# Optimization experiments

Hardware: AMD Instinct MI355X
Metric: run time of the kernel (lower is better)

## Reference

```python
import jax, jax.numpy as jnp
import numpy as np
from jax import lax

LATENT = 64
NUM_EMB = 512
BETA = 0.25
DN = ('NCHW', 'OIHW', 'NCHW')


def conv(x, w, b, stride, pad):
    y = lax.conv_general_dilated(x, w, (stride, stride), [(pad, pad), (pad, pad)],
                                 dimension_numbers=DN)
    return y + b[None, :, None, None]


def tconv(x, w, b, stride, pad, opad):
    # torch ConvTranspose2d(k=3, stride, padding=pad, output_padding=opad)
    # == dilated conv with lhs_dilation=stride, padding (k-1-pad, k-1-pad+opad),
    #    spatially-flipped kernel. w is stored OIHW (out, in, kh, kw).
    k = w.shape[2]
    lo, hi = k - 1 - pad, k - 1 - pad + opad
    y = lax.conv_general_dilated(x, w[:, :, ::-1, ::-1], (1, 1), [(lo, hi), (lo, hi)],
                                 lhs_dilation=(stride, stride), dimension_numbers=DN)
    return y + b[None, :, None, None]


def vector_quantize(z, codebook):
    # z: (B, D, H, W); codebook: (K, D)
    B, D, H, W = z.shape
    flat = z.transpose(0, 2, 3, 1).reshape(-1, D)  # (BHW, D)
    d = (jnp.sum(flat ** 2, axis=1, keepdims=True)
         + jnp.sum(codebook ** 2, axis=1)
         - 2.0 * flat @ codebook.T)  # (BHW, K)
    idx = jnp.argmin(d, axis=1)
    q = codebook[idx].reshape(B, H, W, D).transpose(0, 3, 1, 2)  # (B, D, H, W)
    commitment = jnp.mean((lax.stop_gradient(q) - z) ** 2)
    codebook_loss = jnp.mean((q - lax.stop_gradient(z)) ** 2)
    loss = BETA * commitment + codebook_loss
    q_ste = z + lax.stop_gradient(q - z)  # straight-through estimator
    return q_ste, loss


def setup_inputs() -> dict:
    key = jax.random.key(0)
    ks = jax.random.split(key, 16)
    f32 = jnp.float32
    inp = {
        'x': jax.random.uniform(ks[0], (1024, 1, 50, 50), dtype=f32),
        'enc_w1': jax.random.normal(ks[1], (32, 1, 3, 3), f32) * 0.1,
        'enc_b1': jnp.zeros((32,), f32),
        'enc_w2': jax.random.normal(ks[2], (64, 32, 3, 3), f32) * 0.05,
        'enc_b2': jnp.zeros((64,), f32),
        'enc_w3': jax.random.normal(ks[3], (LATENT, 64, 1, 1), f32) * 0.1,
        'enc_b3': jnp.zeros((LATENT,), f32),
        'codebook': jax.random.uniform(ks[4], (NUM_EMB, LATENT), dtype=f32),
        'dec_w1': jax.random.normal(ks[5], (64, LATENT, 3, 3), f32) * 0.05,
        'dec_b1': jnp.zeros((64,), f32),
        'dec_w2': jax.random.normal(ks[6], (32, 64, 3, 3), f32) * 0.05,
        'dec_b2': jnp.zeros((32,), f32),
        'dec_w3': jax.random.normal(ks[7], (1, 32, 3, 3), f32) * 0.05,
        'dec_b3': jnp.zeros((1,), f32),
    }
    return inp


def reference(x, enc_w1, enc_b1, enc_w2, enc_b2, enc_w3, enc_b3, codebook,
              dec_w1, dec_b1, dec_w2, dec_b2, dec_w3, dec_b3):
    # encoder: (B,1,50,50) -> (B,LATENT,13,13)
    h = jax.nn.relu(conv(x, enc_w1, enc_b1, 2, 1))
    h = jax.nn.relu(conv(h, enc_w2, enc_b2, 2, 1))
    z = conv(h, enc_w3, enc_b3, 1, 0)
    q, vq_loss = vector_quantize(z, codebook)
    # decoder: 13 -> 25 -> 50
    h = jax.nn.relu(tconv(q, dec_w1, dec_b1, 2, 1, 0))
    h = jax.nn.relu(tconv(h, dec_w2, dec_b2, 2, 1, 1))
    x_recon = jax.nn.sigmoid(conv(h, dec_w3, dec_b3, 1, 1))
    return x_recon, vq_loss
```

## Files before the change

### kernel.cpp

```cpp
#include <hip/hip_runtime.h>
#include <math.h>


typedef __attribute__((ext_vector_type(8))) short s8v;
typedef __attribute__((ext_vector_type(4))) float f4v;
typedef __attribute__((ext_vector_type(4))) int i4v;

__device__ inline unsigned short f2bf(float f) {
    unsigned u = __builtin_bit_cast(unsigned, f);
    return (unsigned short)((u + 0x7fffu + ((u >> 16) & 1u)) >> 16);
}
__device__ inline float bf2f(unsigned short h) {
    return __builtin_bit_cast(float, ((unsigned)h) << 16);
}

__global__ __launch_bounds__(64) void k_zero(float* __restrict__ p) {
    if (threadIdx.x == 0 && blockIdx.x == 0) *p = 0.f;
}

__global__ __launch_bounds__(256) void k_prep_cn(const float* __restrict__ cb,
                                                 float* __restrict__ cn) {
    int k = blockIdx.x * 256 + threadIdx.x;
    const float* r = cb + k * 64;
    float s = 0.f;
#pragma unroll
    for (int c = 0; c < 64; ++c) s += r[c] * r[c];
    cn[k] = s;
}
__global__ __launch_bounds__(256) void k_prep_cbm(const float* __restrict__ cb,
                                                  unsigned short* __restrict__ o) {
    int i = blockIdx.x * 256 + threadIdx.x;
    int j = i & 7, lane = (i >> 3) & 63;
    int kc = (i >> 9) % 6, nt = (i >> 9) / 6;
    int n = nt * 16 + (lane & 15);
    int k = kc * 32 + ((lane >> 4) << 3) + j;
    int seg = k >> 6, kk = k & 63;
    float c = cb[n * 64 + kk];
    unsigned short ch = f2bf(c);
    o[i] = (seg == 1) ? f2bf(c - bf2f(ch)) : ch;
}
__global__ __launch_bounds__(256) void k_prep_B2n(const float* __restrict__ w,
                                                  unsigned short* __restrict__ o) {
    int i = blockIdx.x * 256 + threadIdx.x;
    if (i >= 55296) return;
    int j = i & 7, lane = (i >> 3) & 63;
    int kc = (i >> 9) % 27, nt = (i >> 9) / 27;
    int k = kc * 32 + ((lane >> 4) << 3) + j;
    int co = nt * 16 + (lane & 15);
    int part = (k < 288) ? 0 : (k < 576) ? 1 : 0;
    int kk = (k < 288) ? k : (k < 576) ? k - 288 : k - 576;
    int tap = kk >> 5, ci = kk & 31;
    float v = w[(co * 32 + ci) * 9 + tap];
    unsigned short hi = f2bf(v);
    o[i] = part ? f2bf(v - bf2f(hi)) : hi;
}
__global__ __launch_bounds__(256) void k_prep_B3(const float* __restrict__ w,
                                                 unsigned short* __restrict__ o) {
    int i = blockIdx.x * 256 + threadIdx.x;
    if (i >= 12288) return;
    int j = i & 7, lane = (i >> 3) & 63;
    int kc = (i >> 9) % 6, nt = (i >> 9) / 6;
    int k = kc * 32 + ((lane >> 4) << 3) + j;
    int n = nt * 16 + (lane & 15);
    int part = (k < 64) ? 0 : (k < 128) ? 1 : 0;
    int kk = (k < 64) ? k : (k < 128) ? k - 64 : k - 128;
    float v = w[n * 64 + kk];
    unsigned short hi = f2bf(v);
    o[i] = part ? f2bf(v - bf2f(hi)) : hi;
}
__global__ __launch_bounds__(256) void k_prep_B1(const float* __restrict__ w,
                                                 unsigned short* __restrict__ o) {
    int i = blockIdx.x * 256 + threadIdx.x;
    int j = i & 7, l = (i >> 3) & 63, kc = (i >> 9) & 7, nt = i >> 12;
    int n = nt * 16 + (l & 15), k = kc * 32 + (l >> 4) * 8 + j;
    int cls = n >> 6, co = n & 63, p = k >> 6, ci = k & 63;
    int jh = -1, jw = -1;
    if (cls == 0)      { if (p == 0) { jh = 1; jw = 1; } }
    else if (cls == 1) { if (p == 1) { jh = 1; jw = 0; } else if (p == 0) { jh = 1; jw = 2; } }
    else if (cls == 2) { if (p == 2) { jh = 0; jw = 1; } else if (p == 0) { jh = 2; jw = 1; } }
    else { if (p == 3) { jh = 0; jw = 0; } else if (p == 2) { jh = 0; jw = 2; }
           else if (p == 1) { jh = 2; jw = 0; } else { jh = 2; jw = 2; } }
    float v = (jh >= 0) ? w[((co * 64 + ci) * 3 + jh) * 3 + jw] : 0.f;
    o[i] = f2bf(v);
}
__global__ __launch_bounds__(256) void k_prep_B2(const float* __restrict__ w,
                                                 unsigned short* __restrict__ o) {
    int i = blockIdx.x * 256 + threadIdx.x;
    int j = i & 7, l = (i >> 3) & 63, kc = (i >> 9) & 7, nt = i >> 12;
    int n = nt * 16 + (l & 15), k = kc * 32 + (l >> 4) * 8 + j;
    int cls = n >> 5, co = n & 31, p = k >> 6, ci = k & 63;
    int jh = -1, jw = -1;
    if (cls == 0)      { if (p == 0) { jh = 1; jw = 1; } }
    else if (cls == 1) { if (p == 1) { jh = 1; jw = 0; } else if (p == 0) { jh = 1; jw = 2; } }
    else if (cls == 2) { if (p == 2) { jh = 0; jw = 1; } else if (p == 0) { jh = 2; jw = 1; } }
    else { if (p == 3) { jh = 0; jw = 0; } else if (p == 2) { jh = 0; jw = 2; }
           else if (p == 1) { jh = 2; jw = 0; } else { jh = 2; jw = 2; } }
    float v = (jh >= 0) ? w[((co * 64 + ci) * 3 + jh) * 3 + jw] : 0.f;
    o[i] = f2bf(v);
}

__global__ __launch_bounds__(256) void k_conv1(const float* __restrict__ x,
                                               const float* __restrict__ w,
                                               const float* __restrict__ b,
                                               float* __restrict__ h1, int total) {
    __shared__ float4 wl4[72];
    float* wl = (float*)wl4;
    int tid = threadIdx.x;
    for (int t = tid; t < 288; t += 256) {
        int tap = t >> 5, co = t & 31;
        wl[t] = w[co * 9 + tap];
    }
    __syncthreads();
    int pix = blockIdx.x * 256 + tid;
    if (pix >= total) return;
    int n = pix / 625, p = pix % 625, oh = p / 25, ow = p % 25;
    const float* xp = x + (size_t)n * 2500;
    float4 a[8];
#pragma unroll
    for (int j = 0; j < 8; ++j) a[j] = ((const float4*)b)[j];
#pragma unroll
    for (int kh = 0; kh < 3; ++kh) {
        int ih = 2 * oh - 1 + kh;
        if ((unsigned)ih >= 50u) continue;
#pragma unroll
        for (int kw = 0; kw < 3; ++kw) {
            int iw = 2 * ow - 1 + kw;
            if ((unsigned)iw >= 50u) continue;
            float v = xp[ih * 50 + iw];
            int tap = kh * 3 + kw;
#pragma unroll
            for (int j = 0; j < 8; ++j) {
                float4 ww = wl4[tap * 8 + j];
                a[j].x += v * ww.x; a[j].y += v * ww.y;
                a[j].z += v * ww.z; a[j].w += v * ww.w;
            }
        }
    }
    float4* op = (float4*)(h1 + (size_t)pix * 32);
#pragma unroll
    for (int j = 0; j < 8; ++j) {
        float4 r;
        r.x = fmaxf(a[j].x, 0.f); r.y = fmaxf(a[j].y, 0.f);
        r.z = fmaxf(a[j].z, 0.f); r.w = fmaxf(a[j].w, 0.f);
        op[j] = r;
    }
}

__global__ __launch_bounds__(256) void k_enc_m(const float* __restrict__ h1,
                                               const unsigned short* __restrict__ B2n,
                                               const unsigned short* __restrict__ B3,
                                               const float* __restrict__ b2,
                                               const float* __restrict__ b3,
                                               float* __restrict__ z, int npix) {
    __shared__ short a1[16 * 872];
    __shared__ short a2[16 * 200];
    __shared__ float cz[16 * 68];
    int tid = threadIdx.x, blk = blockIdx.x;
    {
        int m = tid >> 4, chunk = tid & 15;
        if (chunk < 9) {
            int pix = blk * 16 + m;
            float4 v[8];
            const float4 zero = {0.f, 0.f, 0.f, 0.f};
            bool ok = false;
            if (pix < npix) {
                int n = pix / 169, p = pix % 169, oh = p / 13, ow = p % 13;
                int kh = chunk / 3, kw = chunk % 3;
                int ih = 2 * oh - 1 + kh, iw = 2 * ow - 1 + kw;
                ok = ((unsigned)ih < 25u) && ((unsigned)iw < 25u);
                if (ok) {
                    const float4* ip = (const float4*)(h1 + (((size_t)n * 25 + ih) * 25 + iw) * 32);
#pragma unroll
                    for (int c4 = 0; c4 < 8; ++c4) v[c4] = ip[c4];
                }
            }
            if (!ok) {
#pragma unroll
                for (int c4 = 0; c4 < 8; ++c4) v[c4] = zero;
            }
            unsigned short hi[32], lo[32];
#pragma unroll
            for (int c4 = 0; c4 < 8; ++c4) {
                float vv[4] = {v[c4].x, v[c4].y, v[c4].z, v[c4].w};
#pragma unroll
                for (int e = 0; e < 4; ++e) {
                    int ci = c4 * 4 + e;
                    unsigned short h = f2bf(vv[e]);
                    hi[ci] = h;
                    lo[ci] = f2bf(vv[e] - bf2f(h));
                }
            }
            short* row = a1 + m * 872 + chunk * 32;
            i4v* d0 = (i4v*)row;
            i4v* d1 = (i4v*)(row + 288);
            i4v* d2 = (i4v*)(row + 576);
#pragma unroll
            for (int g = 0; g < 4; ++g) {
                i4v ph, pl;
#pragma unroll
                for (int e = 0; e < 4; ++e) {
                    int b0 = g * 8 + e * 2;
                    ph[e] = (int)((unsigned)hi[b0] | ((unsigned)hi[b0 + 1] << 16));
                    pl[e] = (int)((unsigned)lo[b0] | ((unsigned)lo[b0 + 1] << 16));
                }
                d0[g] = ph; d1[g] = ph; d2[g] = pl;
            }
        }
    }
    __syncthreads();
    int wave = tid >> 6, lane = tid & 63;
    int arow1 = (lane & 15) * 872 + (lane >> 4) * 8;
    f4v acc = (f4v){0.f, 0.f, 0.f, 0.f};
#pragma unroll
    for (int kc = 0; kc < 27; ++kc) {
        s8v a = *(const s8v*)(a1 + arow1 + kc * 32);
        s8v b = *(const s8v*)((const short*)B2n + ((size_t)((wave * 27 + kc) * 64 + lane)) * 8);
        acc = __builtin_amdgcn_mfma_f32_16x16x32_bf16(a, b, acc, 0, 0, 0);
    }
    {
        float bv = b2[wave * 16 + (lane & 15)];
        int n = wave * 16 + (lane & 15);
#pragma unroll
        for (int r = 0; r < 4; ++r) {
            int m = (lane >> 4) * 4 + r;
            float h = fmaxf(acc[r] + bv, 0.f);
            unsigned short hh = f2bf(h);
            unsigned short ll = f2bf(h - bf2f(hh));
            a2[m * 200 + n] = (short)hh;
            a2[m * 200 + 64 + n] = (short)hh;
            a2[m * 200 + 128 + n] = (short)ll;
        }
    }
    __syncthreads();
    int arow2 = (lane & 15) * 200 + (lane >> 4) * 8;
    f4v acc2 = (f4v){0.f, 0.f, 0.f, 0.f};
#pragma unroll
    for (int kc = 0; kc < 6; ++kc) {
        s8v a = *(const s8v*)(a2 + arow2 + kc * 32);
        s8v b = *(const s8v*)((const short*)B3 + ((size_t)((wave * 6 + kc) * 64 + lane)) * 8);
        acc2 = __builtin_amdgcn_mfma_f32_16x16x32_bf16(a, b, acc2, 0, 0, 0);
    }
    {
        float bv = b3[wave * 16 + (lane & 15)];
        int n = wave * 16 + (lane & 15);
#pragma unroll
        for (int r = 0; r < 4; ++r) {
            int m = (lane >> 4) * 4 + r;
            cz[m * 68 + n] = acc2[r] + bv;
        }
    }
    __syncthreads();
    {
        int m = tid >> 4, c4 = tid & 15;
        int pix = blk * 16 + m;
        if (pix < npix) {
            float4 v = *(float4*)(cz + m * 68 + c4 * 4);
            *(float4*)(z + (size_t)pix * 64 + c4 * 4) = v;
        }
    }
}

__global__ __launch_bounds__(256) void k_vq_m(const float* __restrict__ z,
                                              const float* __restrict__ cb,
                                              const unsigned short* __restrict__ cbm,
                                              const float* __restrict__ cn,
                                              float* __restrict__ q,
                                              float* __restrict__ loss, int npix) {
    __shared__ short a_lds[32 * 200];
    __shared__ float reds[4 * 32];
    __shared__ int   redk[4 * 32];
    __shared__ int   bkf[32];
    __shared__ float lred[4];
    int tid = threadIdx.x, blk = blockIdx.x;
    {
        int m = tid >> 3, p = tid & 7;
        int pix = blk * 32 + m;
        unsigned short zh[8], zl[8];
        if (pix < npix) {
            const float* src = z + (size_t)pix * 64 + p * 8;
#pragma unroll
            for (int v = 0; v < 8; ++v) {
                float f = src[v];
                unsigned short h = f2bf(f);
                zh[v] = h; zl[v] = f2bf(f - bf2f(h));
            }
        } else {
#pragma unroll
            for (int v = 0; v < 8; ++v) { zh[v] = 0; zl[v] = 0; }
        }
        unsigned ph[4], pl[4];
#pragma unroll
        for (int v = 0; v < 4; ++v) {
            ph[v] = (unsigned)zh[2 * v] | ((unsigned)zh[2 * v + 1] << 16);
            pl[v] = (unsigned)zl[2 * v] | ((unsigned)zl[2 * v + 1] << 16);
        }
        short* row = a_lds + m * 200;
        i4v vh = (i4v){(int)ph[0], (int)ph[1], (int)ph[2], (int)ph[3]};
        i4v vl = (i4v){(int)pl[0], (int)pl[1], (int)pl[2], (int)pl[3]};
        *(i4v*)(row + p * 8) = vh;
        *(i4v*)(row + 64 + p * 8) = vh;
        *(i4v*)(row + 128 + p * 8) = vl;
    }
    __syncthreads();
    int wave = tid >> 6, lane = tid & 63;
    s8v af[2][6];
#pragma unroll
    for (int mt = 0; mt < 2; ++mt) {
        int arow = (mt * 16 + (lane & 15)) * 200 + (lane >> 4) * 8;
#pragma unroll
        for (int kc = 0; kc < 6; ++kc)
            af[mt][kc] = *(const s8v*)(a_lds + arow + kc * 32);
    }
    float bd[2][4];
    int bk[2][4];
#pragma unroll
    for (int mt = 0; mt < 2; ++mt)
#pragma unroll
        for (int r = 0; r < 4; ++r) { bd[mt][r] = 3.4e38f; bk[mt][r] = 0; }
#pragma unroll 2
    for (int nt = 0; nt < 8; ++nt) {
        int ntg = wave * 8 + nt;
        s8v bf[6];
#pragma unroll
        for (int kc = 0; kc < 6; ++kc)
            bf[kc] = *(const s8v*)((const short*)cbm + ((size_t)((ntg * 6 + kc) * 64 + lane)) * 8);
        f4v acc0 = (f4v){0.f, 0.f, 0.f, 0.f};
        f4v acc1 = (f4v){0.f, 0.f, 0.f, 0.f};
#pragma unroll
        for (int kc = 0; kc < 6; ++kc) {
            acc0 = __builtin_amdgcn_mfma_f32_16x16x32_bf16(af[0][kc], bf[kc], acc0, 0, 0, 0);
            acc1 = __builtin_amdgcn_mfma_f32_16x16x32_bf16(af[1][kc], bf[kc], acc1, 0, 0, 0);
        }
        int kcol = ntg * 16 + (lane & 15);
        float cnk = cn[kcol];
#pragma unroll
        for (int r = 0; r < 4; ++r) {
            float d0 = cnk - 2.f * acc0[r];
            if (d0 < bd[0][r]) { bd[0][r] = d0; bk[0][r] = kcol; }
            float d1 = cnk - 2.f * acc1[r];
            if (d1 < bd[1][r]) { bd[1][r] = d1; bk[1][r] = kcol; }
        }
    }
#pragma unroll
    for (int off = 1; off < 16; off <<= 1) {
#pragma unroll
        for (int mt = 0; mt < 2; ++mt)
#pragma unroll
            for (int r = 0; r < 4; ++r) {
                float od = __shfl_xor(bd[mt][r], off);
                int ok = __shfl_xor(bk[mt][r], off);
                if (od < bd[mt][r] || (od == bd[mt][r] && ok < bk[mt][r])) {
                    bd[mt][r] = od; bk[mt][r] = ok;
                }
            }
    }
    if ((lane & 15) == 0) {
#pragma unroll
        for (int mt = 0; mt < 2; ++mt)
#pragma unroll
            for (int r = 0; r < 4; ++r) {
                int m = mt * 16 + (lane >> 4) * 4 + r;
                reds[wave * 32 + m] = bd[mt][r];
                redk[wave * 32 + m] = bk[mt][r];
            }
    }
    __syncthreads();
    if (tid < 32) {
        float d0 = reds[tid]; int k0 = redk[tid];
#pragma unroll
        for (int w = 1; w < 4; ++w) {
            float dw = reds[w * 32 + tid]; int kw = redk[w * 32 + tid];
            if (dw < d0 || (dw == d0 && kw < k0)) { d0 = dw; k0 = kw; }
        }
        bkf[tid] = k0;
    }
    __syncthreads();
    float lsum = 0.f;
#pragma unroll
    for (int it = 0; it < 2; ++it) {
        int m = tid >> 3, c4 = (tid & 7) + it * 8;
        int pix = blk * 32 + m;
        if (pix < npix) {
            int k0 = bkf[m];
            float4 cq = ((const float4*)cb)[(size_t)k0 * 16 + c4];
            float4 zz = ((const float4*)(z + (size_t)pix * 64))[c4];
            float dx = cq.x - zz.x, dy = cq.y - zz.y, dz = cq.z - zz.z, dw = cq.w - zz.w;
            lsum += dx * dx + dy * dy + dz * dz + dw * dw;
            ((float4*)(q + (size_t)pix * 64))[c4] = cq;
        }
    }
#pragma unroll
    for (int off = 32; off > 0; off >>= 1) lsum += __shfl_down(lsum, off);
    if ((tid & 63) == 0) lred[tid >> 6] = lsum;
    __syncthreads();
    if (tid == 0) {
        float t = lred[0] + lred[1] + lred[2] + lred[3];
        atomicAdd(loss, t * (1.25f / 11075584.f));
    }
}

__global__ __launch_bounds__(256) void k_tconv1_m(const float* __restrict__ q,
                                                  const unsigned short* __restrict__ wB,
                                                  const float* __restrict__ bias,
                                                  unsigned short* __restrict__ d1,
                                                  int nquad) {
    __shared__ short a_lds[32 * 264];
    __shared__ short c_lds[32 * 264];
    int tid = threadIdx.x, blk = blockIdx.x;
#pragma unroll
    for (int pass = 0; pass < 4; ++pass) {
        int idx = tid + pass * 256;
        int m = idx >> 5, sub = idx & 31;
        int qg = blk * 32 + m;
        int p = sub >> 3, ci0 = (sub & 7) * 8;
        unsigned short t8[8];
        bool have = false;
        if (qg < nquad) {
            int img = qg / 169, r = qg % 169, qm = r / 13, qw = r % 13;
            int sm = qm + (p >> 1), sw = qw + (p & 1);
            if (sm < 13 && sw < 13) {
                const float* src = q + (((size_t)img * 13 + sm) * 13 + sw) * 64 + ci0;
#pragma unroll
                for (int v = 0; v < 8; ++v) t8[v] = f2bf(src[v]);
                have = true;
            }
        }
        if (!have) {
#pragma unroll
            for (int v = 0; v < 8; ++v) t8[v] = 0;
        }
        i4v pk;
#pragma unroll
        for (int e = 0; e < 4; ++e)
            pk[e] = (int)((unsigned)t8[2 * e] | ((unsigned)t8[2 * e + 1] << 16));
        *(i4v*)(a_lds + m * 264 + sub * 8) = pk;
    }
    __syncthreads();
    int wave = tid >> 6, lane = tid & 63;
    f4v acc[2][4];
#pragma unroll
    for (int mt = 0; mt < 2; ++mt)
#pragma unroll
        for (int i = 0; i < 4; ++i) acc[mt][i] = (f4v){0.f, 0.f, 0.f, 0.f};
    float bv[4];
#pragma unroll
    for (int i = 0; i < 4; ++i) bv[i] = bias[((wave * 4 + i) * 16 + (lane & 15)) & 63];
#pragma unroll
    for (int kc = 0; kc < 8; ++kc) {
        s8v a0 = *(const s8v*)(a_lds + ((lane & 15)) * 264 + (lane >> 4) * 8 + kc * 32);
        s8v a1 = *(const s8v*)(a_lds + (16 + (lane & 15)) * 264 + (lane >> 4) * 8 + kc * 32);
#pragma unroll
        for (int i = 0; i < 4; ++i) {
            int nt = wave * 4 + i;
            s8v b = *(const s8v*)((const short*)wB + ((size_t)((nt * 8 + kc) * 64 + lane)) * 8);
            acc[0][i] = __builtin_amdgcn_mfma_f32_16x16x32_bf16(a0, b, acc[0][i], 0, 0, 0);
            acc[1][i] = __builtin_amdgcn_mfma_f32_16x16x32_bf16(a1, b, acc[1][i], 0, 0, 0);
        }
    }
#pragma unroll
    for (int mt = 0; mt < 2; ++mt)
#pragma unroll
        for (int i = 0; i < 4; ++i) {
            int n = (wave * 4 + i) * 16 + (lane & 15);
#pragma unroll
            for (int r2 = 0; r2 < 4; ++r2) {
                int m = mt * 16 + (lane >> 4) * 4 + r2;
                float v = fmaxf(acc[mt][i][r2] + bv[i], 0.f);
                c_lds[m * 264 + n] = (short)f2bf(v);
            }
        }
    __syncthreads();
#pragma unroll
    for (int pass = 0; pass < 4; ++pass) {
        int ch = tid + pass * 256;
        int m = ch >> 5, cpart = ch & 31;
        int qg = blk * 32 + m;
        if (qg >= nquad) continue;
        int img = qg / 169, r = qg % 169, qm = r / 13, qw = r % 13;
        int cls = cpart >> 3, co8 = (cpart & 7) * 8;
        int oh = 2 * qm + (cls >> 1), ow = 2 * qw + (cls & 1);
        if (oh >= 25 || ow >= 25) continue;
        i4v val = *(i4v*)(c_lds + m * 264 + cls * 64 + co8);
        *(i4v*)(d1 + (((size_t)img * 25 + oh) * 25 + ow) * 64 + co8) = val;
    }
}

__global__ __launch_bounds__(256) void k_tconv2_m(const unsigned short* __restrict__ d1,
                                                  const unsigned short* __restrict__ wB,
                                                  const float* __restrict__ bias,
                                                  unsigned short* __restrict__ d2,
                                                  int nquad) {
    __shared__ short a_lds[32 * 264];
    __shared__ short c_lds[32 * 136];
    int tid = threadIdx.x, blk = blockIdx.x;
#pragma unroll
    for (int pass = 0; pass < 4; ++pass) {
        int idx = tid + pass * 256;
        int m = idx >> 5, sub = idx & 31;
        int qg = blk * 32 + m;
        int p = sub >> 3, ci0 = (sub & 7) * 8;
        i4v v = (i4v){0, 0, 0, 0};
        if (qg < nquad) {
            int img = qg / 625, r = qg % 625, qm = r / 25, qw = r % 25;
            int sm = qm + (p >> 1), sw = qw + (p & 1);
            if (sm < 25 && sw < 25)
                v = *(const i4v*)(d1 + (((size_t)img * 25 + sm) * 25 + sw) * 64 + ci0);
        }
        *(i4v*)(a_lds + m * 264 + sub * 8) = v;
    }
    __syncthreads();
    int wave = tid >> 6, lane = tid & 63;
    f4v acc[2][2];
#pragma unroll
    for (int mt = 0; mt < 2; ++mt)
#pragma unroll
        for (int i = 0; i < 2; ++i) acc[mt][i] = (f4v){0.f, 0.f, 0.f, 0.f};
    float bv[2];
#pragma unroll
    for (int i = 0; i < 2; ++i) bv[i] = bias[((wave * 2 + i) * 16 + (lane & 15)) & 31];
#pragma unroll
    for (int kc = 0; kc < 8; ++kc) {
        s8v a0 = *(const s8v*)(a_lds + ((lane & 15)) * 264 + (lane >> 4) * 8 + kc * 32);
        s8v a1 = *(const s8v*)(a_lds + (16 + (lane & 15)) * 264 + (lane >> 4) * 8 + kc * 32);
#pragma unroll
        for (int i = 0; i < 2; ++i) {
            int nt = wave * 2 + i;
            s8v b = *(const s8v*)((const short*)wB + ((size_t)((nt * 8 + kc) * 64 + lane)) * 8);
            acc[0][i] = __builtin_amdgcn_mfma_f32_16x16x32_bf16(a0, b, acc[0][i], 0, 0, 0);
            acc[1][i] = __builtin_amdgcn_mfma_f32_16x16x32_bf16(a1, b, acc[1][i], 0, 0, 0);
        }
    }
#pragma unroll
    for (int mt = 0; mt < 2; ++mt)
#pragma unroll
        for (int i = 0; i < 2; ++i) {
            int n = (wave * 2 + i) * 16 + (lane & 15);
#pragma unroll
            for (int r2 = 0; r2 < 4; ++r2) {
                int m = mt * 16 + (lane >> 4) * 4 + r2;
                float v = fmaxf(acc[mt][i][r2] + bv[i], 0.f);
                c_lds[m * 136 + n] = (short)f2bf(v);
            }
        }
    __syncthreads();
#pragma unroll
    for (int pass = 0; pass < 2; ++pass) {
        int ch = tid + pass * 256;
        int m = ch >> 4, cpart = ch & 15;
        int qg = blk * 32 + m;
        if (qg >= nquad) continue;
        int img = qg / 625, r = qg % 625, qm = r / 25, qw = r % 25;
        int cls = cpart >> 2, co8 = (cpart & 3) * 8;
        int oh = 2 * qm + (cls >> 1), ow = 2 * qw + (cls & 1);
        i4v val = *(i4v*)(c_lds + m * 136 + cls * 32 + co8);
        *(i4v*)(d2 + (((size_t)img * 50 + oh) * 50 + ow) * 32 + co8) = val;
    }
}

__global__ __launch_bounds__(256) void k_convf(const unsigned short* __restrict__ in,
                                               const float* __restrict__ w,
                                               const float* __restrict__ b,
                                               float* __restrict__ out, int total) {
    __shared__ float wl[288];
    int tid = threadIdx.x;
    for (int t = tid; t < 288; t += 256) {
        int tap = t >> 5, ci = t & 31;
        wl[t] = w[ci * 9 + tap];
    }
    __syncthreads();
    int pix = blockIdx.x * 256 + tid;
    if (pix >= total) return;
    int n = pix / 2500, p = pix % 2500, oh = p / 50, ow = p % 50;
    float acc = b[0];
#pragma unroll
    for (int kh = 0; kh < 3; ++kh) {
        int ih = oh - 1 + kh;
        if ((unsigned)ih >= 50u) continue;
#pragma unroll
        for (int kw = 0; kw < 3; ++kw) {
            int iw = ow - 1 + kw;
            if ((unsigned)iw >= 50u) continue;
            const float* wt = wl + (kh * 3 + kw) * 32;
            const i4v* ip4 = (const i4v*)(in + (((size_t)n * 50 + ih) * 50 + iw) * 32);
#pragma unroll
            for (int c8 = 0; c8 < 4; ++c8) {
                i4v u = ip4[c8];
#pragma unroll
                for (int e = 0; e < 4; ++e) {
                    unsigned uu = (unsigned)u[e];
                    float x0 = __builtin_bit_cast(float, uu << 16);
                    float x1 = __builtin_bit_cast(float, uu & 0xffff0000u);
                    acc = fmaf(x0, wt[c8 * 8 + e * 2], acc);
                    acc = fmaf(x1, wt[c8 * 8 + e * 2 + 1], acc);
                }
            }
        }
    }
    out[pix] = 1.f / (1.f + expf(-acc));
}

extern "C" void kernel_launch(void* const* d_in, const int* in_sizes, int n_in,
                              void* d_out, int out_size, void* d_ws, size_t ws_size,
                              hipStream_t stream) {
    const float* x   = (const float*)d_in[0];
    const float* ew1 = (const float*)d_in[1];
    const float* eb1 = (const float*)d_in[2];
    const float* ew2 = (const float*)d_in[3];
    const float* eb2 = (const float*)d_in[4];
    const float* ew3 = (const float*)d_in[5];
    const float* eb3 = (const float*)d_in[6];
    const float* cb  = (const float*)d_in[7];
    const float* dw1 = (const float*)d_in[8];
    const float* db1 = (const float*)d_in[9];
    const float* dw2 = (const float*)d_in[10];
    const float* db2 = (const float*)d_in[11];
    const float* dw3 = (const float*)d_in[12];
    const float* db3 = (const float*)d_in[13];
    float* out = (float*)d_out;
    float* loss = out + 2560000;

    float* ws = (float*)d_ws;
    float* cn = ws;
    unsigned short* wB1  = (unsigned short*)(ws + 512);
    unsigned short* wB2  = (unsigned short*)(ws + 33280);
    unsigned short* wB2n = (unsigned short*)(ws + 49664);
    unsigned short* wB3  = (unsigned short*)(ws + 77312);
    unsigned short* cbm  = (unsigned short*)(ws + 83456);
    const size_t tw_floats = 132608;

    const int B = 1024;
    const size_t A_per = 40000, B_per = 20000;
    size_t avail = (ws_size / 4 > tw_floats) ? ws_size / 4 - tw_floats : 0;
    int BC = (int)(avail / (A_per + B_per));
    if (BC > B) BC = B;
    if (BC < 1) BC = 1;
    float* regA = ws + tw_floats;
    float* regB = regA + (size_t)BC * A_per;

    k_zero<<<1, 64, 0, stream>>>(loss);
    k_prep_cn <<<2, 256, 0, stream>>>(cb, cn);
    k_prep_cbm<<<384, 256, 0, stream>>>(cb, cbm);
    k_prep_B2n<<<216, 256, 0, stream>>>(ew2, wB2n);
    k_prep_B3 <<<48, 256, 0, stream>>>(ew3, wB3);
    k_prep_B1 <<<256, 256, 0, stream>>>(dw1, wB1);
    k_prep_B2 <<<128, 256, 0, stream>>>(dw2, wB2);

    for (int n0 = 0; n0 < B; n0 += BC) {
        int bc = (B - n0 < BC) ? (B - n0) : BC;
        const float* xch = x + (size_t)n0 * 2500;

        int t1 = bc * 625;
        k_conv1<<<(t1 + 255) / 256, 256, 0, stream>>>(xch, ew1, eb1, regA, t1);

        int npix = bc * 169;
        k_enc_m<<<(npix + 15) / 16, 256, 0, stream>>>(regA, wB2n, wB3, eb2, eb3, regB, npix);

        k_vq_m<<<(npix + 31) / 32, 256, 0, stream>>>(regB, cb, cbm, cn, regA, loss, npix);

        unsigned short* d1 = (unsigned short*)regB;
        k_tconv1_m<<<(npix + 31) / 32, 256, 0, stream>>>(regA, wB1, db1, d1, npix);

        int nq2 = bc * 625;
        unsigned short* d2 = (unsigned short*)regA;
        k_tconv2_m<<<(nq2 + 31) / 32, 256, 0, stream>>>(d1, wB2, db2, d2, nq2);

        int t6 = bc * 2500;
        k_convf<<<(t6 + 255) / 256, 256, 0, stream>>>(d2, dw3, db3, out + (size_t)n0 * 2500, t6);
    }
}
```

Measured before the change: 513.6 us.

## Merge weight-prep kernels into one launch and widen VQ tile to 64 pixels

Combines seven small preparation kernels (codebook split, weight packing, codebook norms, loss zeroing) into a single kernel with index-range dispatch, removing several launch overheads. The VQ kernel now processes 64 pixels per block instead of 32. Each codebook B-fragment loaded from global memory is reused across four MFMA row tiles instead of two, which halves total codebook traffic. The cost is more registers and LDS per block, and the nt loop unrolling drops to 1, which can lower occupancy.

```diff
diff --git a/kernel.cpp b/kernel.cpp
--- a/kernel.cpp
+++ b/kernel.cpp
@@ -14,89 +14,83 @@
     return __builtin_bit_cast(float, ((unsigned)h) << 16);
 }
 
-__global__ __launch_bounds__(64) void k_zero(float* __restrict__ p) {
-    if (threadIdx.x == 0 && blockIdx.x == 0) *p = 0.f;
-}
-
-__global__ __launch_bounds__(256) void k_prep_cn(const float* __restrict__ cb,
-                                                 float* __restrict__ cn) {
-    int k = blockIdx.x * 256 + threadIdx.x;
-    const float* r = cb + k * 64;
-    float s = 0.f;
-#pragma unroll
-    for (int c = 0; c < 64; ++c) s += r[c] * r[c];
-    cn[k] = s;
-}
-__global__ __launch_bounds__(256) void k_prep_cbm(const float* __restrict__ cb,
-                                                  unsigned short* __restrict__ o) {
+__global__ __launch_bounds__(256) void k_prep_all(
+        const float* __restrict__ cb,  const float* __restrict__ ew2,
+        const float* __restrict__ ew3, const float* __restrict__ dw1,
+        const float* __restrict__ dw2,
+        unsigned short* __restrict__ cbm, unsigned short* __restrict__ wB2n,
+        unsigned short* __restrict__ wB1, unsigned short* __restrict__ wB2,
+        unsigned short* __restrict__ wB3, float* __restrict__ cn,
+        float* __restrict__ loss) {
     int i = blockIdx.x * 256 + threadIdx.x;
-    int j = i & 7, lane = (i >> 3) & 63;
-    int kc = (i >> 9) % 6, nt = (i >> 9) / 6;
-    int n = nt * 16 + (lane & 15);
-    int k = kc * 32 + ((lane >> 4) << 3) + j;
-    int seg = k >> 6, kk = k & 63;
-    float c = cb[n * 64 + kk];
-    unsigned short ch = f2bf(c);
-    o[i] = (seg == 1) ? f2bf(c - bf2f(ch)) : ch;
-}
-__global__ __launch_bounds__(256) void k_prep_B2n(const float* __restrict__ w,
-                                                  unsigned short* __restrict__ o) {
-    int i = blockIdx.x * 256 + threadIdx.x;
-    if (i >= 55296) return;
-    int j = i & 7, lane = (i >> 3) & 63;
-    int kc = (i >> 9) % 27, nt = (i >> 9) / 27;
-    int k = kc * 32 + ((lane >> 4) << 3) + j;
-    int co = nt * 16 + (lane & 15);
-    int part = (k < 288) ? 0 : (k < 576) ? 1 : 0;
-    int kk = (k < 288) ? k : (k < 576) ? k - 288 : k - 576;
-    int tap = kk >> 5, ci = kk & 31;
-    float v = w[(co * 32 + ci) * 9 + tap];
-    unsigned short hi = f2bf(v);
-    o[i] = part ? f2bf(v - bf2f(hi)) : hi;
-}
-__global__ __launch_bounds__(256) void k_prep_B3(const float* __restrict__ w,
-                                                 unsigned short* __restrict__ o) {
-    int i = blockIdx.x * 256 + threadIdx.x;
-    if (i >= 12288) return;
-    int j = i & 7, lane = (i >> 3) & 63;
-    int kc = (i >> 9) % 6, nt = (i >> 9) / 6;
-    int k = kc * 32 + ((lane >> 4) << 3) + j;
-    int n = nt * 16 + (lane & 15);
-    int part = (k < 64) ? 0 : (k < 128) ? 1 : 0;
-    int kk = (k < 64) ? k : (k < 128) ? k - 64 : k - 128;
-    float v = w[n * 64 + kk];
-    unsigned short hi = f2bf(v);
-    o[i] = part ? f2bf(v - bf2f(hi)) : hi;
-}
-__global__ __launch_bounds__(256) void k_prep_B1(const float* __restrict__ w,
-                                                 unsigned short* __restrict__ o) {
-    int i = blockIdx.x * 256 + threadIdx.x;
-    int j = i & 7, l = (i >> 3) & 63, kc = (i >> 9) & 7, nt = i >> 12;
-    int n = nt * 16 + (l & 15), k = kc * 32 + (l >> 4) * 8 + j;
-    int cls = n >> 6, co = n & 63, p = k >> 6, ci = k & 63;
-    int jh = -1, jw = -1;
-    if (cls == 0)      { if (p == 0) { jh = 1; jw = 1; } }
-    else if (cls == 1) { if (p == 1) { jh = 1; jw = 0; } else if (p == 0) { jh = 1; jw = 2; } }
-    else if (cls == 2) { if (p == 2) { jh = 0; jw = 1; } else if (p == 0) { jh = 2; jw = 1; } }
-    else { if (p == 3) { jh = 0; jw = 0; } else if (p == 2) { jh = 0; jw = 2; }
-           else if (p == 1) { jh = 2; jw = 0; } else { jh = 2; jw = 2; } }
-    float v = (jh >= 0) ? w[((co * 64 + ci) * 3 + jh) * 3 + jw] : 0.f;
-    o[i] = f2bf(v);
-}
-__global__ __launch_bounds__(256) void k_prep_B2(const float* __restrict__ w,
-                                                 unsigned short* __restrict__ o) {
-    int i = blockIdx.x * 256 + threadIdx.x;
-    int j = i & 7, l = (i >> 3) & 63, kc = (i >> 9) & 7, nt = i >> 12;
-    int n = nt * 16 + (l & 15), k = kc * 32 + (l >> 4) * 8 + j;
-    int cls = n >> 5, co = n & 31, p = k >> 6, ci = k & 63;
-    int jh = -1, jw = -1;
-    if (cls == 0)      { if (p == 0) { jh = 1; jw = 1; } }
-    else if (cls == 1) { if (p == 1) { jh = 1; jw = 0; } else if (p == 0) { jh = 1; jw = 2; } }
-    else if (cls == 2) { if (p == 2) { jh = 0; jw = 1; } else if (p == 0) { jh = 2; jw = 1; } }
-    else { if (p == 3) { jh = 0; jw = 0; } else if (p == 2) { jh = 0; jw = 2; }
-           else if (p == 1) { jh = 2; jw = 0; } else { jh = 2; jw = 2; } }
-    float v = (jh >= 0) ? w[((co * 64 + ci) * 3 + jh) * 3 + jw] : 0.f;
-    o[i] = f2bf(v);
+    if (i < 98304) {
+        int j = i & 7, lane = (i >> 3) & 63;
+        int kc = (i >> 9) % 6, nt = (i >> 9) / 6;
+        int n = nt * 16 + (lane & 15);
+        int k = kc * 32 + ((lane >> 4) << 3) + j;
+        int seg = k >> 6, kk = k & 63;
+        float c = cb[n * 64 + kk];
+        unsigned short ch = f2bf(c);
+        cbm[i] = (seg == 1) ? f2bf(c - bf2f(ch)) : ch;
+    } else if (i < 153600) {
+        int q = i - 98304;
+        int j = q & 7, lane = (q >> 3) & 63;
+        int kc = (q >> 9) % 27, nt = (q >> 9) / 27;
+        int k = kc * 32 + ((lane >> 4) << 3) + j;
+        int co = nt * 16 + (lane & 15);
+        int part = (k < 288) ? 0 : (k < 576) ? 1 : 0;
+        int kk = (k < 288) ? k : (k < 576) ? k - 288 : k - 576;
+        int tap = kk >> 5, ci = kk & 31;
+        float v = ew2[(co * 32 + ci) * 9 + tap];
+        unsigned short hi = f2bf(v);
+        wB2n[q] = part ? f2bf(v - bf2f(hi)) : hi;
+    } else if (i < 219136) {
+        int q = i - 153600;
+        int j = q & 7, l = (q >> 3) & 63, kc = (q >> 9) & 7, nt = q >> 12;
+        int n = nt * 16 + (l & 15), k = kc * 32 + (l >> 4) * 8 + j;
+        int cls = n >> 6, co = n & 63, p = k >> 6, ci = k & 63;
+        int jh = -1, jw = -1;
+        if (cls == 0)      { if (p == 0) { jh = 1; jw = 1; } }
+        else if (cls == 1) { if (p == 1) { jh = 1; jw = 0; } else if (p == 0) { jh = 1; jw = 2; } }
+        else if (cls == 2) { if (p == 2) { jh = 0; jw = 1; } else if (p == 0) { jh = 2; jw = 1; } }
+        else { if (p == 3) { jh = 0; jw = 0; } else if (p == 2) { jh = 0; jw = 2; }
+               else if (p == 1) { jh = 2; jw = 0; } else { jh = 2; jw = 2; } }
+        float v = (jh >= 0) ? dw1[((co * 64 + ci) * 3 + jh) * 3 + jw] : 0.f;
+        wB1[q] = f2bf(v);
+    } else if (i < 251904) {
+        int q = i - 219136;
+        int j = q & 7, l = (q >> 3) & 63, kc = (q >> 9) & 7, nt = q >> 12;
+        int n = nt * 16 + (l & 15), k = kc * 32 + (l >> 4) * 8 + j;
+        int cls = n >> 5, co = n & 31, p = k >> 6, ci = k & 63;
+        int jh = -1, jw = -1;
+        if (cls == 0)      { if (p == 0) { jh = 1; jw = 1; } }
+        else if (cls == 1) { if (p == 1) { jh = 1; jw = 0; } else if (p == 0) { jh = 1; jw = 2; } }
+        else if (cls == 2) { if (p == 2) { jh = 0; jw = 1; } else if (p == 0) { jh = 2; jw = 1; } }
+        else { if (p == 3) { jh = 0; jw = 0; } else if (p == 2) { jh = 0; jw = 2; }
+               else if (p == 1) { jh = 2; jw = 0; } else { jh = 2; jw = 2; } }
+        float v = (jh >= 0) ? dw2[((co * 64 + ci) * 3 + jh) * 3 + jw] : 0.f;
+        wB2[q] = f2bf(v);
+    } else if (i < 264192) {
+        int q = i - 251904;
+        int j = q & 7, lane = (q >> 3) & 63;
+        int kc = (q >> 9) % 6, nt = (q >> 9) / 6;
+        int k = kc * 32 + ((lane >> 4) << 3) + j;
+        int n = nt * 16 + (lane & 15);
+        int part = (k < 64) ? 0 : (k < 128) ? 1 : 0;
+        int kk = (k < 64) ? k : (k < 128) ? k - 64 : k - 128;
+        float v = ew3[n * 64 + kk];
+        unsigned short hi = f2bf(v);
+        wB3[q] = part ? f2bf(v - bf2f(hi)) : hi;
+    } else if (i < 264704) {
+        int k = i - 264192;
+        const float* r = cb + k * 64;
+        float s = 0.f;
+#pragma unroll
+        for (int c = 0; c < 64; ++c) s += r[c] * r[c];
+        cn[k] = s;
+    } else if (i == 264704) {
+        *loss = 0.f;
+    }
 }
 
 __global__ __launch_bounds__(256) void k_conv1(const float* __restrict__ x,
@@ -266,15 +260,17 @@
                                               const float* __restrict__ cn,
                                               float* __restrict__ q,
                                               float* __restrict__ loss, int npix) {
-    __shared__ short a_lds[32 * 200];
-    __shared__ float reds[4 * 32];
-    __shared__ int   redk[4 * 32];
-    __shared__ int   bkf[32];
+    __shared__ short a_lds[64 * 200];
+    __shared__ float reds[4 * 64];
+    __shared__ int   redk[4 * 64];
+    __shared__ int   bkf[64];
     __shared__ float lred[4];
     int tid = threadIdx.x, blk = blockIdx.x;
-    {
-        int m = tid >> 3, p = tid & 7;
-        int pix = blk * 32 + m;
+#pragma unroll
+    for (int it = 0; it < 2; ++it) {
+        int idx = tid + it * 256;
+        int m = idx >> 3, p = idx & 7;
+        int pix = blk * 64 + m;
         unsigned short zh[8], zl[8];
         if (pix < npix) {
             const float* src = z + (size_t)pix * 64 + p * 8;
@@ -303,48 +299,50 @@
     }
     __syncthreads();
     int wave = tid >> 6, lane = tid & 63;
-    s8v af[2][6];
-#pragma unroll
-    for (int mt = 0; mt < 2; ++mt) {
+    s8v af[4][6];
+#pragma unroll
+    for (int mt = 0; mt < 4; ++mt) {
         int arow = (mt * 16 + (lane & 15)) * 200 + (lane >> 4) * 8;
 #pragma unroll
         for (int kc = 0; kc < 6; ++kc)
             af[mt][kc] = *(const s8v*)(a_lds + arow + kc * 32);
     }
-    float bd[2][4];
-    int bk[2][4];
-#pragma unroll
-    for (int mt = 0; mt < 2; ++mt)
+    float bd[4][4];
+    int bk[4][4];
+#pragma unroll
+    for (int mt = 0; mt < 4; ++mt)
 #pragma unroll
         for (int r = 0; r < 4; ++r) { bd[mt][r] = 3.4e38f; bk[mt][r] = 0; }
-#pragma unroll 2
+#pragma unroll 1
     for (int nt = 0; nt < 8; ++nt) {
         int ntg = wave * 8 + nt;
         s8v bf[6];
 #pragma unroll
         for (int kc = 0; kc < 6; ++kc)
             bf[kc] = *(const s8v*)((const short*)cbm + ((size_t)((ntg * 6 + kc) * 64 + lane)) * 8);
-        f4v acc0 = (f4v){0.f, 0.f, 0.f, 0.f};
-        f4v acc1 = (f4v){0.f, 0.f, 0.f, 0.f};
+        f4v acc[4];
+#pragma unroll
+        for (int mt = 0; mt < 4; ++mt) acc[mt] = (f4v){0.f, 0.f, 0.f, 0.f};
 #pragma unroll
         for (int kc = 0; kc < 6; ++kc) {
-            acc0 = __builtin_amdgcn_mfma_f32_16x16x32_bf16(af[0][kc], bf[kc], acc0, 0, 0, 0);
-            acc1 = __builtin_amdgcn_mfma_f32_16x16x32_bf16(af[1][kc], bf[kc], acc1, 0, 0, 0);
+#pragma unroll
+            for (int mt = 0; mt < 4; ++mt)
+                acc[mt] = __builtin_amdgcn_mfma_f32_16x16x32_bf16(af[mt][kc], bf[kc], acc[mt], 0, 0, 0);
         }
         int kcol = ntg * 16 + (lane & 15);
         float cnk = cn[kcol];
 #pragma unroll
-        for (int r = 0; r < 4; ++r) {
-            float d0 = cnk - 2.f * acc0[r];
-            if (d0 < bd[0][r]) { bd[0][r] = d0; bk[0][r] = kcol; }
-            float d1 = cnk - 2.f * acc1[r];
-            if (d1 < bd[1][r]) { bd[1][r] = d1; bk[1][r] = kcol; }
-        }
+        for (int mt = 0; mt < 4; ++mt)
+#pragma unroll
+            for (int r = 0; r < 4; ++r) {
+                float d = cnk - 2.f * acc[mt][r];
+                if (d < bd[mt][r]) { bd[mt][r] = d; bk[mt][r] = kcol; }
+            }
     }
 #pragma unroll
     for (int off = 1; off < 16; off <<= 1) {
 #pragma unroll
-        for (int mt = 0; mt < 2; ++mt)
+        for (int mt = 0; mt < 4; ++mt)
 #pragma unroll
             for (int r = 0; r < 4; ++r) {
                 float od = __shfl_xor(bd[mt][r], off);
@@ -356,20 +354,20 @@
     }
     if ((lane & 15) == 0) {
 #pragma unroll
-        for (int mt = 0; mt < 2; ++mt)
+        for (int mt = 0; mt < 4; ++mt)
 #pragma unroll
             for (int r = 0; r < 4; ++r) {
                 int m = mt * 16 + (lane >> 4) * 4 + r;
-                reds[wave * 32 + m] = bd[mt][r];
-                redk[wave * 32 + m] = bk[mt][r];
-            }
-    }
-    __syncthreads();
-    if (tid < 32) {
+                reds[wave * 64 + m] = bd[mt][r];
+                redk[wave * 64 + m] = bk[mt][r];
+            }
+    }
+    __syncthreads();
+    if (tid < 64) {
         float d0 = reds[tid]; int k0 = redk[tid];
 #pragma unroll
         for (int w = 1; w < 4; ++w) {
-            float dw = reds[w * 32 + tid]; int kw = redk[w * 32 + tid];
+            float dw = reds[w * 64 + tid]; int kw = redk[w * 64 + tid];
             if (dw < d0 || (dw == d0 && kw < k0)) { d0 = dw; k0 = kw; }
         }
         bkf[tid] = k0;
@@ -377,9 +375,10 @@
     __syncthreads();
     float lsum = 0.f;
 #pragma unroll
-    for (int it = 0; it < 2; ++it) {
-        int m = tid >> 3, c4 = (tid & 7) + it * 8;
-        int pix = blk * 32 + m;
+    for (int it = 0; it < 4; ++it) {
+        int idx = tid + it * 256;
+        int m = idx >> 4, c4 = idx & 15;
+        int pix = blk * 64 + m;
         if (pix < npix) {
             int k0 = bkf[m];
             float4 cq = ((const float4*)cb)[(size_t)k0 * 16 + c4];
@@ -637,13 +636,8 @@
     float* regA = ws + tw_floats;
     float* regB = regA + (size_t)BC * A_per;
 
-    k_zero<<<1, 64, 0, stream>>>(loss);
-    k_prep_cn <<<2, 256, 0, stream>>>(cb, cn);
-    k_prep_cbm<<<384, 256, 0, stream>>>(cb, cbm);
-    k_prep_B2n<<<216, 256, 0, stream>>>(ew2, wB2n);
-    k_prep_B3 <<<48, 256, 0, stream>>>(ew3, wB3);
-    k_prep_B1 <<<256, 256, 0, stream>>>(dw1, wB1);
-    k_prep_B2 <<<128, 256, 0, stream>>>(dw2, wB2);
+    k_prep_all<<<1035, 256, 0, stream>>>(cb, ew2, ew3, dw1, dw2,
+                                         cbm, wB2n, wB1, wB2, wB3, cn, loss);
 
     for (int n0 = 0; n0 < B; n0 += BC) {
         int bc = (B - n0 < BC) ? (B - n0) : BC;
@@ -655,7 +649,7 @@
         int npix = bc * 169;
         k_enc_m<<<(npix + 15) / 16, 256, 0, stream>>>(regA, wB2n, wB3, eb2, eb3, regB, npix);
 
-        k_vq_m<<<(npix + 31) / 32, 256, 0, stream>>>(regB, cb, cbm, cn, regA, loss, npix);
+        k_vq_m<<<(npix + 63) / 64, 256, 0, stream>>>(regB, cb, cbm, cn, regA, loss, npix);
 
         unsigned short* d1 = (unsigned short*)regB;
         k_tconv1_m<<<(npix + 31) / 32, 256, 0, stream>>>(regA, wB1, db1, d1, npix);
```

Result: no change. 503.7 us (-1.9%).
